# Kernel tuning notes

Measured on AMD Instinct MI355X. Metric: run time of the kernel, lower is better.

The kernel has to match this reference:

```python
import jax, jax.numpy as jnp
import numpy as np

NEG_SLOPE = 0.2

def gat_conv(x, src, dst, W, a_src, a_dst, b, num_nodes, concat):
    # PyG GATConv (add_self_loops already applied to src/dst).
    H, C = a_src.shape
    h = (x @ W).reshape(-1, H, C)                      # [N,H,C]
    s = jnp.einsum('nhc,hc->nh', h, a_src)             # per-node src score
    d = jnp.einsum('nhc,hc->nh', h, a_dst)             # per-node dst score
    e = jax.nn.leaky_relu(s[src] + d[dst], NEG_SLOPE)  # [E,H]
    emax = jax.lax.stop_gradient(
        jax.ops.segment_max(e, dst, num_segments=num_nodes))  # [N,H]
    ex = jnp.exp(e - emax[dst])
    denom = jax.ops.segment_sum(ex, dst, num_segments=num_nodes)
    alpha = ex / denom[dst]                            # segment softmax over in-edges
    msg = h[src] * alpha[:, :, None]                   # [E,H,C]
    out = jax.ops.segment_sum(msg, dst, num_segments=num_nodes)
    out = out.reshape(num_nodes, H * C) if concat else out.mean(axis=1)
    return out + b

def setup_inputs() -> dict:
    key = jax.random.key(0)
    ks = jax.random.split(key, 20)
    N, E, F = 50000, 400000, 256
    x = jax.random.normal(ks[0], (N, F), dtype=jnp.float32)
    edge_index = jax.random.randint(ks[1], (2, E), 0, N, dtype=jnp.int64)
    def p(k, shape):
        return (jax.random.normal(k, shape, dtype=jnp.float32) * 0.1)
    inp = {'x': x, 'edge_index': edge_index}
    # conv1: 256 -> 8x32 ; conv2: 256 -> 4x32 ; conv3: 128 -> 2x32 ; conv4: 64 -> 1x32
    dims = [(256, 8, 32), (256, 4, 32), (128, 2, 32), (64, 1, 32)]
    ki = 2
    for i, (fin, H, C) in enumerate(dims, start=1):
        inp[f'W{i}'] = p(ks[ki], (fin, H * C)); ki += 1
        inp[f'a_src{i}'] = p(ks[ki], (H, C)); ki += 1
        inp[f'a_dst{i}'] = p(ks[ki], (H, C)); ki += 1
        bdim = H * C if i < 4 else C
        inp[f'b{i}'] = jnp.zeros((bdim,), dtype=jnp.float32)
    return inp

def reference(x, edge_index, W1, a_src1, a_dst1, b1, W2, a_src2, a_dst2, b2,
              W3, a_src3, a_dst3, b3, W4, a_src4, a_dst4, b4):
    N = x.shape[0]
    loops = jnp.arange(N, dtype=edge_index.dtype)
    src = jnp.concatenate([edge_index[0], loops])
    dst = jnp.concatenate([edge_index[1], loops])
    h = jax.nn.elu(gat_conv(x, src, dst, W1, a_src1, a_dst1, b1, N, True))
    h = jax.nn.elu(gat_conv(h, src, dst, W2, a_src2, a_dst2, b2, N, True))
    h = gat_conv(h, src, dst, W3, a_src3, a_dst3, b3, N, True)
    h = jax.nn.elu(h)
    h = gat_conv(h, src, dst, W4, a_src4, a_dst4, b4, N, False)
    return jax.nn.log_softmax(h, axis=1)
```

## Files before the change

kernel.cpp:

```cpp
#include <hip/hip_runtime.h>
#include <hip/hip_bf16.h>

#define LRELU_SLOPE 0.2f

typedef __attribute__((ext_vector_type(8))) short short8;
typedef __attribute__((ext_vector_type(4))) float f32x4;

__device__ __forceinline__ unsigned short bf16r(float f) {
    unsigned int u = __builtin_bit_cast(unsigned int, f);
    u += 0x7fffu + ((u >> 16) & 1u);
    return (unsigned short)(u >> 16);
}
__device__ __forceinline__ float bf2f(unsigned short u) {
    return __builtin_bit_cast(float, (unsigned int)u << 16);
}


#define WTOT 108544

__global__ void k_pre(const float* __restrict__ Wa, const float* __restrict__ Wb,
                      const float* __restrict__ Wc, const float* __restrict__ Wd,
                      unsigned short* __restrict__ Ta, unsigned short* __restrict__ Tb,
                      unsigned short* __restrict__ Tc, unsigned short* __restrict__ Td,
                      const int* __restrict__ ei, int* __restrict__ cnt, int E, int N) {
    int gid = blockIdx.x * blockDim.x + threadIdx.x;
    if (gid < WTOT) {
        int id = gid;
        const float* W; unsigned short* T; int K, Nc;
        if (id < 65536)       { W = Wa; T = Ta; K = 256; Nc = 256; }
        else if (id < 98304)  { id -= 65536;  W = Wb; T = Tb; K = 256; Nc = 128; }
        else if (id < 106496) { id -= 98304;  W = Wc; T = Tc; K = 128; Nc = 64; }
        else                  { id -= 106496; W = Wd; T = Td; K = 64;  Nc = 32; }
        int n = id / K, k = id % K;
        T[id] = bf16r(W[(long)k * Nc + n]);
        return;
    }
    int e = gid - WTOT;
    if (e >= E + N) return;
    int dst = (e < E) ? ei[E + e] : (e - E);
    atomicAdd(&cnt[dst], 1);
}


__global__ void k_scan_blk(const int* __restrict__ cnt, int* __restrict__ offs,
                           int* __restrict__ bsum, int N) {
    __shared__ int temp[1024];
    int t = threadIdx.x;
    int gi = blockIdx.x * 1024 + t;
    int v = (gi < N) ? cnt[gi] : 0;
    temp[t] = v;
    __syncthreads();
    for (int o = 1; o < 1024; o <<= 1) {
        int x = (t >= o) ? temp[t - o] : 0;
        __syncthreads();
        temp[t] += x;
        __syncthreads();
    }
    if (gi < N) offs[gi] = temp[t] - v;
    if (t == 1023) bsum[blockIdx.x] = temp[1023];
}

__global__ void k_scan(const int* __restrict__ cnt, int* __restrict__ offs, int N) {
    __shared__ int temp[1024];
    __shared__ int carry_s;
    int t = threadIdx.x;
    if (t == 0) carry_s = 0;
    __syncthreads();
    for (int base = 0; base < N; base += 1024) {
        int v = (base + t < N) ? cnt[base + t] : 0;
        temp[t] = v;
        __syncthreads();
        for (int o = 1; o < 1024; o <<= 1) {
            int x = (t >= o) ? temp[t - o] : 0;
            __syncthreads();
            temp[t] += x;
            __syncthreads();
        }
        int incl = temp[t];
        int carry = carry_s;
        if (base + t < N) offs[base + t] = carry + incl - v;
        __syncthreads();
        if (t == 1023) carry_s = carry + temp[1023];
        __syncthreads();
    }
    if (t == 0) offs[N] = carry_s;
}

__global__ void k_scan_add(int* __restrict__ offs, const int* __restrict__ bpre,
                           int* __restrict__ wp, int N, int nb) {
    int gi = blockIdx.x * blockDim.x + threadIdx.x;
    if (gi < N) {
        int v = offs[gi] + bpre[gi >> 10];
        offs[gi] = v;
        wp[gi] = v;
    } else if (gi == N) {
        offs[N] = bpre[nb];
    }
}

__global__ void k_scatter(const int* __restrict__ ei, int* __restrict__ wp,
                          int* __restrict__ adj, int E, int N) {
    int e = blockIdx.x * blockDim.x + threadIdx.x;
    if (e >= E + N) return;
    int srcn = (e < E) ? ei[e] : (e - E);
    int dst  = (e < E) ? ei[E + e] : (e - E);
    int pos = atomicAdd(&wp[dst], 1);
    adj[pos] = srcn;
}


#define PSTR 40

template<int BN, bool F32A>
__global__ __launch_bounds__(256) void k_mgemm(const void* __restrict__ Ain,
                                               const unsigned short* __restrict__ WT,
                                               unsigned short* __restrict__ Cb,
                                               const float* __restrict__ a_src,
                                               const float* __restrict__ a_dst,
                                               float* __restrict__ sbuf,
                                               float* __restrict__ dbuf,
                                               int M, int Nc, int K, int H) {
    constexpr int NBF = BN / 16;
    constexpr int BCH = BN / 64;
    constexpr int SP  = BN + 8;
    constexpr int CPR = BN / 32;
    constexpr int STAGE = 64 * PSTR + BN * PSTR;
    constexpr int EPIL  = 64 * SP;
    constexpr int LBSZ  = STAGE > EPIL ? STAGE : EPIL;
    __shared__ __align__(16) unsigned short LB[LBSZ];
    unsigned short* As = LB;
    unsigned short* Bs = LB + 64 * PSTR;

    int t = threadIdx.x;
    int wv = t >> 6, l = t & 63;
    int bm = blockIdx.y * 64, bn = blockIdx.x * BN;

    f32x4 acc[NBF];
#pragma unroll
    for (int j = 0; j < NBF; ++j) acc[j] = (f32x4){0.f, 0.f, 0.f, 0.f};

    int ar = t >> 2, akc = t & 3;
    int grA = min(bm + ar, M - 1);
    int bc[BCH], gcB[BCH];
#pragma unroll
    for (int i = 0; i < BCH; ++i) {
        bc[i] = (t >> 2) + i * 64;
        gcB[i] = min(bn + bc[i], Nc - 1);
    }

    int row_in = l & 15, quad = l >> 4;
    const short8* apf = (const short8*)&As[(wv * 16 + row_in) * PSTR + quad * 8];
    const short8* bpf[NBF];
#pragma unroll
    for (int f = 0; f < NBF; ++f)
        bpf[f] = (const short8*)&Bs[(f * 16 + row_in) * PSTR + quad * 8];

    const float* Af = (const float*)Ain;
    const unsigned short* Ab = (const unsigned short*)Ain;

    float4 af0, af1, af0n, af1n;
    short8 ab8, ab8n;
    short8 bb[BCH], bbn[BCH];

    if constexpr (F32A) {
        const float4* p = (const float4*)&Af[(long)grA * K + akc * 8];
        af0 = p[0]; af1 = p[1];
    } else {
        ab8 = *(const short8*)&Ab[(long)grA * K + akc * 8];
    }
#pragma unroll
    for (int i = 0; i < BCH; ++i)
        bb[i] = *(const short8*)&WT[(long)gcB[i] * K + akc * 8];

    for (int k0 = 0; k0 < K; k0 += 32) {
        short8 av;
        if constexpr (F32A) {
            av[0] = (short)bf16r(af0.x); av[1] = (short)bf16r(af0.y);
            av[2] = (short)bf16r(af0.z); av[3] = (short)bf16r(af0.w);
            av[4] = (short)bf16r(af1.x); av[5] = (short)bf16r(af1.y);
            av[6] = (short)bf16r(af1.z); av[7] = (short)bf16r(af1.w);
        } else {
            av = ab8;
        }
        *(short8*)&As[ar * PSTR + akc * 8] = av;
#pragma unroll
        for (int i = 0; i < BCH; ++i)
            *(short8*)&Bs[bc[i] * PSTR + akc * 8] = bb[i];
        __syncthreads();

        int kn = k0 + 32;
        if (kn < K) {
            if constexpr (F32A) {
                const float4* p = (const float4*)&Af[(long)grA * K + kn + akc * 8];
                af0n = p[0]; af1n = p[1];
            } else {
                ab8n = *(const short8*)&Ab[(long)grA * K + kn + akc * 8];
            }
#pragma unroll
            for (int i = 0; i < BCH; ++i)
                bbn[i] = *(const short8*)&WT[(long)gcB[i] * K + kn + akc * 8];
        }

        short8 a0 = *apf;
#pragma unroll
        for (int f = 0; f < NBF; ++f) {
            short8 b = *bpf[f];
            acc[f] = __builtin_amdgcn_mfma_f32_16x16x32_bf16(a0, b, acc[f], 0, 0, 0);
        }
        __syncthreads();

        af0 = af0n; af1 = af1n; ab8 = ab8n;
#pragma unroll
        for (int i = 0; i < BCH; ++i) bb[i] = bbn[i];
    }

#pragma unroll
    for (int r = 0; r < 4; ++r)
#pragma unroll
        for (int ct = 0; ct < NBF; ++ct)
            LB[(wv * 16 + quad * 4 + r) * SP + ct * 16 + row_in] = bf16r(acc[ct][r]);
    __syncthreads();

    int rr = t / CPR, cc = t % CPR;
    if (rr < 64) {
        int grow = bm + rr;
        int colb = bn + cc * 32;
        if (grow < M && colb < Nc) {
            const unsigned short* ep = &LB[rr * SP + cc * 32];
            short8 v0 = *(const short8*)(ep);
            short8 v1 = *(const short8*)(ep + 8);
            short8 v2 = *(const short8*)(ep + 16);
            short8 v3 = *(const short8*)(ep + 24);
            unsigned short* cp = &Cb[(long)grow * Nc + colb];
            *(short8*)(cp)      = v0;
            *(short8*)(cp + 8)  = v1;
            *(short8*)(cp + 16) = v2;
            *(short8*)(cp + 24) = v3;
            int hd = colb >> 5;
            const float* ap = a_src + hd * 32;
            const float* dp = a_dst + hd * 32;
            float ss = 0.f, dd = 0.f;
#pragma unroll
            for (int u = 0; u < 8; ++u) {
                float va = bf2f((unsigned short)v0[u]); ss += va * ap[u];      dd += va * dp[u];
                float vb = bf2f((unsigned short)v1[u]); ss += vb * ap[8 + u];  dd += vb * dp[8 + u];
                float vc = bf2f((unsigned short)v2[u]); ss += vc * ap[16 + u]; dd += vc * dp[16 + u];
                float vd = bf2f((unsigned short)v3[u]); ss += vd * ap[24 + u]; dd += vd * dp[24 + u];
            }
            sbuf[(long)grow * H + hd] = ss;
            dbuf[(long)grow * H + hd] = dd;
        }
    }
}


template<int ACT>
__global__ void k_aggf(const unsigned short* __restrict__ h, const float* __restrict__ s,
                       const float* __restrict__ dsc, const int* __restrict__ offs,
                       const int* __restrict__ adj, const float* __restrict__ bias,
                       unsigned short* __restrict__ out16, float* __restrict__ out32,
                       int N, int H) {
    const int C8 = 4;
    long tid = (long)blockIdx.x * blockDim.x + threadIdx.x;
    int HC8 = H * C8;
    if (tid >= (long)N * HC8) return;
    int c8 = (int)(tid % C8);
    int hh = (int)((tid / C8) % H);
    int n  = (int)(tid / HC8);
    int beg = offs[n], end = offs[n + 1];
    float dn = dsc[n * H + hh];
    int HC = HC8 * 8;
    int coff = hh * 32 + c8 * 8;

    float denom = 0.f;
    float acc[8];
#pragma unroll
    for (int u = 0; u < 8; ++u) acc[u] = 0.f;

    for (int j = beg; j < end; ++j) {
        int sn = adj[j];
        float e = s[sn * H + hh] + dn;
        e = e > 0.f ? e : LRELU_SLOPE * e;
        float w = __expf(fminf(e, 80.f));
        short8 hv = *(const short8*)(h + (size_t)sn * HC + coff);
        denom += w;
#pragma unroll
        for (int u = 0; u < 8; ++u)
            acc[u] += w * bf2f((unsigned short)hv[u]);
    }

    float inv = 1.0f / denom;
    float o[8];
#pragma unroll
    for (int u = 0; u < 8; ++u) o[u] = acc[u] * inv + bias[coff + u];

    if (ACT == 1) {
        short8 pk;
#pragma unroll
        for (int u = 0; u < 8; ++u) {
            float v = o[u] > 0.f ? o[u] : (__expf(o[u]) - 1.f);
            pk[u] = (short)bf16r(v);
        }
        *(short8*)(out16 + tid * 8) = pk;
    } else {
        float m = o[0];
#pragma unroll
        for (int u = 1; u < 8; ++u) m = fmaxf(m, o[u]);
        m = fmaxf(m, __shfl_xor(m, 1));
        m = fmaxf(m, __shfl_xor(m, 2));
        float ssum = 0.f;
#pragma unroll
        for (int u = 0; u < 8; ++u) ssum += __expf(o[u] - m);
        ssum += __shfl_xor(ssum, 1);
        ssum += __shfl_xor(ssum, 2);
        float lse = m + __logf(ssum);
        float4 lo = {o[0] - lse, o[1] - lse, o[2] - lse, o[3] - lse};
        float4 hi = {o[4] - lse, o[5] - lse, o[6] - lse, o[7] - lse};
        *(float4*)(out32 + tid * 8)     = lo;
        *(float4*)(out32 + tid * 8 + 4) = hi;
    }
}


static inline size_t align_up(size_t x) { return (x + 255) & ~(size_t)255; }

extern "C" void kernel_launch(void* const* d_in, const int* in_sizes, int n_in,
                              void* d_out, int out_size, void* d_ws, size_t ws_size,
                              hipStream_t stream) {
    const float* x   = (const float*)d_in[0];
    const int*   ei  = (const int*)d_in[1];

    const int N = in_sizes[0] / 256;
    const int E = in_sizes[1] / 2;
    const int ET = E + N;
    const int NB = (N + 1023) / 1024;

    size_t off = 0;
    char* ws = (char*)d_ws;
    auto take = [&](size_t bytes) { char* p = ws + off; off += align_up(bytes); return p; };
    int*   offs  = (int*)take((size_t)(N + 1) * 4);
    int*   wp    = (int*)take((size_t)N * 4);
    int*   adj   = (int*)take((size_t)ET * 4);
    int*   bsum  = (int*)take((size_t)(NB + 1) * 4);
    int*   bpre  = (int*)take((size_t)(NB + 1) * 4);
    float* sbuf  = (float*)take((size_t)N * 8 * 4);
    float* dbuf  = (float*)take((size_t)N * 8 * 4);
    unsigned short* Xb = (unsigned short*)take((size_t)N * 256 * 2);
    unsigned short* Yb = (unsigned short*)take((size_t)N * 256 * 2);
    unsigned short* WT0 = (unsigned short*)take((size_t)256 * 256 * 2);
    unsigned short* WT1 = (unsigned short*)take((size_t)256 * 128 * 2);
    unsigned short* WT2 = (unsigned short*)take((size_t)128 * 64 * 2);
    unsigned short* WT3 = (unsigned short*)take((size_t)64 * 32 * 2);
    (void)ws_size;

    hipMemsetAsync(wp, 0, (size_t)N * 4, stream);
    {
        long tot = WTOT + ET;
        k_pre<<<(int)((tot + 255) / 256), 256, 0, stream>>>(
            (const float*)d_in[2], (const float*)d_in[6], (const float*)d_in[10],
            (const float*)d_in[14], WT0, WT1, WT2, WT3, ei, wp, E, N);
        k_scan_blk<<<NB, 1024, 0, stream>>>(wp, offs, bsum, N);
        k_scan<<<1, 1024, 0, stream>>>(bsum, bpre, NB);
        k_scan_add<<<(N + 256) / 256, 256, 0, stream>>>(offs, bpre, wp, N, NB);
        k_scatter<<<(ET + 255) / 256, 256, 0, stream>>>(ei, wp, adj, E, N);
    }

    struct Layer { const float* as; const float* ad; const float* b;
                   const unsigned short* WT; int Fin; int H; };
    Layer layers[4] = {
        {(const float*)d_in[3],  (const float*)d_in[4],  (const float*)d_in[5],  WT0, 256, 8},
        {(const float*)d_in[7],  (const float*)d_in[8],  (const float*)d_in[9],  WT1, 256, 4},
        {(const float*)d_in[11], (const float*)d_in[12], (const float*)d_in[13], WT2, 128, 2},
        {(const float*)d_in[15], (const float*)d_in[16], (const float*)d_in[17], WT3,  64, 1},
    };

    for (int li = 0; li < 4; ++li) {
        Layer& L = layers[li];
        int HC = L.H * 32;
        int K = L.Fin;

        if (li == 0) {
            dim3 grd((HC + 127) / 128, (N + 63) / 64);
            k_mgemm<128, true><<<grd, 256, 0, stream>>>(x, L.WT, Yb, L.as, L.ad,
                                                        sbuf, dbuf, N, HC, K, L.H);
        } else if (HC >= 128) {
            dim3 grd(HC / 128, (N + 63) / 64);
            k_mgemm<128, false><<<grd, 256, 0, stream>>>(Xb, L.WT, Yb, L.as, L.ad,
                                                         sbuf, dbuf, N, HC, K, L.H);
        } else {
            dim3 grd((HC + 63) / 64, (N + 63) / 64);
            k_mgemm<64, false><<<grd, 256, 0, stream>>>(Xb, L.WT, Yb, L.as, L.ad,
                                                        sbuf, dbuf, N, HC, K, L.H);
        }
        {
            long total = (long)N * L.H * 4;
            int nb = (int)((total + 255) / 256);
            if (li < 3)
                k_aggf<1><<<nb, 256, 0, stream>>>(Yb, sbuf, dbuf, offs, adj, L.b,
                                                  Xb, nullptr, N, L.H);
            else
                k_aggf<0><<<nb, 256, 0, stream>>>(Yb, sbuf, dbuf, offs, adj, L.b,
                                                  nullptr, (float*)d_out, N, L.H);
        }
    }
}
```

Baseline: 349.4 us.

## Stage full-K weight tile in LDS once and keep A rows in registers

The GEMM kernel now makes K a template parameter and loads the whole BN×K weight slice into shared memory once per block. Each lane loads its A fragments for all K steps straight from global memory into registers, which removes the per-step LDS staging of A and the two barriers per 32-wide K step. Column tiles shrink (BN 64 or 32), so the grid has more blocks along N, and A rows are re-read by several column blocks. Register use rises because the whole K extent of A is held per lane, which may lower occupancy.

```diff
diff --git a/kernel.cpp b/kernel.cpp
--- a/kernel.cpp
+++ b/kernel.cpp
@@ -109,9 +109,7 @@
 }
 
 
-#define PSTR 40
-
-template<int BN, bool F32A>
+template<int BN, int KT, bool F32A>
 __global__ __launch_bounds__(256) void k_mgemm(const void* __restrict__ Ain,
                                                const unsigned short* __restrict__ WT,
                                                unsigned short* __restrict__ Cb,
@@ -119,106 +117,80 @@
                                                const float* __restrict__ a_dst,
                                                float* __restrict__ sbuf,
                                                float* __restrict__ dbuf,
-                                               int M, int Nc, int K, int H) {
+                                               int M, int Nc, int H) {
+    constexpr int KITER = KT / 32;
+    constexpr int KS  = KT + 8;
     constexpr int NBF = BN / 16;
-    constexpr int BCH = BN / 64;
+    constexpr int CPR = BN / 32;
     constexpr int SP  = BN + 8;
-    constexpr int CPR = BN / 32;
-    constexpr int STAGE = 64 * PSTR + BN * PSTR;
+    constexpr int STAGE = BN * KS;
     constexpr int EPIL  = 64 * SP;
     constexpr int LBSZ  = STAGE > EPIL ? STAGE : EPIL;
     __shared__ __align__(16) unsigned short LB[LBSZ];
-    unsigned short* As = LB;
-    unsigned short* Bs = LB + 64 * PSTR;
 
     int t = threadIdx.x;
     int wv = t >> 6, l = t & 63;
+    int row_in = l & 15, quad = l >> 4;
     int bm = blockIdx.y * 64, bn = blockIdx.x * BN;
 
-    f32x4 acc[NBF];
-#pragma unroll
-    for (int j = 0; j < NBF; ++j) acc[j] = (f32x4){0.f, 0.f, 0.f, 0.f};
-
-    int ar = t >> 2, akc = t & 3;
-    int grA = min(bm + ar, M - 1);
-    int bc[BCH], gcB[BCH];
-#pragma unroll
-    for (int i = 0; i < BCH; ++i) {
-        bc[i] = (t >> 2) + i * 64;
-        gcB[i] = min(bn + bc[i], Nc - 1);
-    }
-
-    int row_in = l & 15, quad = l >> 4;
-    const short8* apf = (const short8*)&As[(wv * 16 + row_in) * PSTR + quad * 8];
-    const short8* bpf[NBF];
-#pragma unroll
-    for (int f = 0; f < NBF; ++f)
-        bpf[f] = (const short8*)&Bs[(f * 16 + row_in) * PSTR + quad * 8];
-
+    int grA = min(bm + wv * 16 + row_in, M - 1);
     const float* Af = (const float*)Ain;
     const unsigned short* Ab = (const unsigned short*)Ain;
-
-    float4 af0, af1, af0n, af1n;
-    short8 ab8, ab8n;
-    short8 bb[BCH], bbn[BCH];
-
+    float4 af0[KITER], af1[KITER];
+    short8 areg[KITER];
     if constexpr (F32A) {
-        const float4* p = (const float4*)&Af[(long)grA * K + akc * 8];
-        af0 = p[0]; af1 = p[1];
+#pragma unroll
+        for (int ki = 0; ki < KITER; ++ki) {
+            const float4* p = (const float4*)&Af[(long)grA * KT + ki * 32 + quad * 8];
+            af0[ki] = p[0];
+            af1[ki] = p[1];
+        }
     } else {
-        ab8 = *(const short8*)&Ab[(long)grA * K + akc * 8];
-    }
-#pragma unroll
-    for (int i = 0; i < BCH; ++i)
-        bb[i] = *(const short8*)&WT[(long)gcB[i] * K + akc * 8];
-
-    for (int k0 = 0; k0 < K; k0 += 32) {
+#pragma unroll
+        for (int ki = 0; ki < KITER; ++ki)
+            areg[ki] = *(const short8*)&Ab[(long)grA * KT + ki * 32 + quad * 8];
+    }
+
+    constexpr int PER = BN * (KT / 8) / 256;
+#pragma unroll
+    for (int i = 0; i < PER; ++i) {
+        int ch = t + i * 256;
+        int col = ch / (KT / 8);
+        int kc  = ch % (KT / 8);
+        int gcol = min(bn + col, Nc - 1);
+        *(short8*)&LB[col * KS + kc * 8] = *(const short8*)&WT[(long)gcol * KT + kc * 8];
+    }
+    __syncthreads();
+
+    f32x4 acc[NBF];
+#pragma unroll
+    for (int j = 0; j < NBF; ++j) acc[j] = (f32x4){0.f, 0.f, 0.f, 0.f};
+
+#pragma unroll
+    for (int ki = 0; ki < KITER; ++ki) {
         short8 av;
         if constexpr (F32A) {
-            av[0] = (short)bf16r(af0.x); av[1] = (short)bf16r(af0.y);
-            av[2] = (short)bf16r(af0.z); av[3] = (short)bf16r(af0.w);
-            av[4] = (short)bf16r(af1.x); av[5] = (short)bf16r(af1.y);
-            av[6] = (short)bf16r(af1.z); av[7] = (short)bf16r(af1.w);
+            float4 f0 = af0[ki], f1 = af1[ki];
+            av[0] = (short)bf16r(f0.x); av[1] = (short)bf16r(f0.y);
+            av[2] = (short)bf16r(f0.z); av[3] = (short)bf16r(f0.w);
+            av[4] = (short)bf16r(f1.x); av[5] = (short)bf16r(f1.y);
+            av[6] = (short)bf16r(f1.z); av[7] = (short)bf16r(f1.w);
         } else {
-            av = ab8;
-        }
-        *(short8*)&As[ar * PSTR + akc * 8] = av;
-#pragma unroll
-        for (int i = 0; i < BCH; ++i)
-            *(short8*)&Bs[bc[i] * PSTR + akc * 8] = bb[i];
-        __syncthreads();
-
-        int kn = k0 + 32;
-        if (kn < K) {
-            if constexpr (F32A) {
-                const float4* p = (const float4*)&Af[(long)grA * K + kn + akc * 8];
-                af0n = p[0]; af1n = p[1];
-            } else {
-                ab8n = *(const short8*)&Ab[(long)grA * K + kn + akc * 8];
-            }
-#pragma unroll
-            for (int i = 0; i < BCH; ++i)
-                bbn[i] = *(const short8*)&WT[(long)gcB[i] * K + kn + akc * 8];
-        }
-
-        short8 a0 = *apf;
+            av = areg[ki];
+        }
 #pragma unroll
         for (int f = 0; f < NBF; ++f) {
-            short8 b = *bpf[f];
-            acc[f] = __builtin_amdgcn_mfma_f32_16x16x32_bf16(a0, b, acc[f], 0, 0, 0);
-        }
-        __syncthreads();
-
-        af0 = af0n; af1 = af1n; ab8 = ab8n;
-#pragma unroll
-        for (int i = 0; i < BCH; ++i) bb[i] = bbn[i];
-    }
+            short8 bv = *(const short8*)&LB[(f * 16 + row_in) * KS + ki * 32 + quad * 8];
+            acc[f] = __builtin_amdgcn_mfma_f32_16x16x32_bf16(av, bv, acc[f], 0, 0, 0);
+        }
+    }
+    __syncthreads();
 
 #pragma unroll
     for (int r = 0; r < 4; ++r)
 #pragma unroll
-        for (int ct = 0; ct < NBF; ++ct)
-            LB[(wv * 16 + quad * 4 + r) * SP + ct * 16 + row_in] = bf16r(acc[ct][r]);
+        for (int f = 0; f < NBF; ++f)
+            LB[(wv * 16 + quad * 4 + r) * SP + f * 16 + row_in] = bf16r(acc[f][r]);
     __syncthreads();
 
     int rr = t / CPR, cc = t % CPR;
@@ -365,42 +337,41 @@
         k_scatter<<<(ET + 255) / 256, 256, 0, stream>>>(ei, wp, adj, E, N);
     }
 
-    struct Layer { const float* as; const float* ad; const float* b;
-                   const unsigned short* WT; int Fin; int H; };
-    Layer layers[4] = {
-        {(const float*)d_in[3],  (const float*)d_in[4],  (const float*)d_in[5],  WT0, 256, 8},
-        {(const float*)d_in[7],  (const float*)d_in[8],  (const float*)d_in[9],  WT1, 256, 4},
-        {(const float*)d_in[11], (const float*)d_in[12], (const float*)d_in[13], WT2, 128, 2},
-        {(const float*)d_in[15], (const float*)d_in[16], (const float*)d_in[17], WT3,  64, 1},
-    };
-
+    const float* as_[4] = {(const float*)d_in[3], (const float*)d_in[7],
+                           (const float*)d_in[11], (const float*)d_in[15]};
+    const float* ad_[4] = {(const float*)d_in[4], (const float*)d_in[8],
+                           (const float*)d_in[12], (const float*)d_in[16]};
+    const float* b_[4]  = {(const float*)d_in[5], (const float*)d_in[9],
+                           (const float*)d_in[13], (const float*)d_in[17]};
+    int H_[4] = {8, 4, 2, 1};
+
+    int gy = (N + 63) / 64;
     for (int li = 0; li < 4; ++li) {
-        Layer& L = layers[li];
-        int HC = L.H * 32;
-        int K = L.Fin;
+        int H = H_[li];
+        int HC = H * 32;
 
         if (li == 0) {
-            dim3 grd((HC + 127) / 128, (N + 63) / 64);
-            k_mgemm<128, true><<<grd, 256, 0, stream>>>(x, L.WT, Yb, L.as, L.ad,
-                                                        sbuf, dbuf, N, HC, K, L.H);
-        } else if (HC >= 128) {
-            dim3 grd(HC / 128, (N + 63) / 64);
-            k_mgemm<128, false><<<grd, 256, 0, stream>>>(Xb, L.WT, Yb, L.as, L.ad,
-                                                         sbuf, dbuf, N, HC, K, L.H);
+            k_mgemm<64, 256, true><<<dim3(4, gy), 256, 0, stream>>>(
+                x, WT0, Yb, as_[0], ad_[0], sbuf, dbuf, N, 256, H);
+        } else if (li == 1) {
+            k_mgemm<64, 256, false><<<dim3(2, gy), 256, 0, stream>>>(
+                Xb, WT1, Yb, as_[1], ad_[1], sbuf, dbuf, N, 128, H);
+        } else if (li == 2) {
+            k_mgemm<64, 128, false><<<dim3(1, gy), 256, 0, stream>>>(
+                Xb, WT2, Yb, as_[2], ad_[2], sbuf, dbuf, N, 64, H);
         } else {
-            dim3 grd((HC + 63) / 64, (N + 63) / 64);
-            k_mgemm<64, false><<<grd, 256, 0, stream>>>(Xb, L.WT, Yb, L.as, L.ad,
-                                                        sbuf, dbuf, N, HC, K, L.H);
+            k_mgemm<32, 64, false><<<dim3(1, gy), 256, 0, stream>>>(
+                Xb, WT3, Yb, as_[3], ad_[3], sbuf, dbuf, N, 32, H);
         }
         {
-            long total = (long)N * L.H * 4;
+            long total = (long)N * H * 4;
             int nb = (int)((total + 255) / 256);
             if (li < 3)
-                k_aggf<1><<<nb, 256, 0, stream>>>(Yb, sbuf, dbuf, offs, adj, L.b,
-                                                  Xb, nullptr, N, L.H);
+                k_aggf<1><<<nb, 256, 0, stream>>>(Yb, sbuf, dbuf, offs, adj, b_[li],
+                                                  Xb, nullptr, N, H);
             else
-                k_aggf<0><<<nb, 256, 0, stream>>>(Yb, sbuf, dbuf, offs, adj, L.b,
-                                                  nullptr, (float*)d_out, N, L.H);
-        }
-    }
-}
+                k_aggf<0><<<nb, 256, 0, stream>>>(Yb, sbuf, dbuf, offs, adj, b_[li],
+                                                  nullptr, (float*)d_out, N, H);
+        }
+    }
+}
```

New measurement: 340.2 us. -2.6%, faster.
